# Optimization experiments

Measured on AMD Instinct MI355X. Metric: run time of the kernel, lower is better.

Reference implementation:

```python
import jax, jax.numpy as jnp
import numpy as np

K = 2            # top-k experts
TEMPERATURE = 1.0
EPS = 1e-9


def setup_inputs() -> dict:
    key = jax.random.key(0)
    k1, k2 = jax.random.split(key)
    B, S, D = 4, 4096, 4096
    G, E = 4, 64
    x = jax.random.normal(k1, (B, S, D), dtype=jnp.float32)
    # stacked gate weights, one [E, D] Linear weight per gate head
    W = jax.random.normal(k2, (G, E, D), dtype=jnp.float32) * 0.02
    return {"x": x, "W": W}


def reference(x, W):
    # per-head logits over experts: [B, S, G, E]; jitter disabled (eval / jitter_noise=0)
    logits = jnp.einsum('bsd,ged->bsge', x, W) * (1.0 / TEMPERATURE)
    probs = jax.nn.softmax(logits, axis=-1)          # softmax per head
    probs_full = probs.mean(axis=2)                  # consensus over heads: [B, S, E]
    topk_vals, idx = jax.lax.top_k(probs_full, K)    # sorted descending, matches aten.topk
    den = jnp.sum(topk_vals, axis=-1, keepdims=True)
    scores = topk_vals / jnp.maximum(den, EPS)       # clamp_min(den, 1e-9)
    pf = jax.lax.stop_gradient(probs_full)           # aux stats under no_grad
    importance = pf.mean(axis=(0, 1))                # [E]
    load = (pf > 0.0).astype(pf.dtype).mean(axis=(0, 1))  # [E]
    return idx, scores, probs_full, importance, load
```

## Files before the change

### kernel.cpp

```cpp
#include <hip/hip_runtime.h>

typedef _Float16 f16x8 __attribute__((ext_vector_type(8)));
typedef float    f32x4 __attribute__((ext_vector_type(4)));

#define MROWS 16384
#define NCOLS 256
#define KDIM  4096
#define BM    128
#define BK    32
#define LDA   40

#define OUT_SCORES 32768
#define OUT_PF     65536
#define OUT_IMP    1114112
#define OUT_LOAD   1114176

__global__ __launch_bounds__(256) void wprep(const float* __restrict__ W,
                                             _Float16* __restrict__ wfHi,
                                             _Float16* __restrict__ wfLo) {
    int t  = blockIdx.x * 256 + threadIdx.x;
    int n  = t >> 9;
    int k8 = t & 511;
    const float* src = W + ((size_t)n * KDIM + (size_t)k8 * 8);
    f16x8 hi, lo;
#pragma unroll
    for (int j = 0; j < 8; ++j) {
        float x = src[j];
        _Float16 h = (_Float16)x;
        hi[j] = h;
        lo[j] = (_Float16)(x - (float)h);
    }
    int NT  = n >> 4;
    int ksg = k8 >> 2;
    int l   = (n & 15) + ((k8 & 3) << 4);
    size_t dst = ((size_t)(ksg * 16 + NT) * 64 + (size_t)l) * 8;
    *(f16x8*)(wfHi + dst) = hi;
    *(f16x8*)(wfLo + dst) = lo;
}

__global__ __launch_bounds__(256, 2) void gemm3(const float* __restrict__ X,
        const _Float16* __restrict__ wfHi, const _Float16* __restrict__ wfLo,
        float* __restrict__ lsplit, int kQ) {
    __shared__ _Float16 aHi[BM * LDA];
    __shared__ _Float16 aLo[BM * LDA];

    const int tid  = threadIdx.x;
    const int lane = tid & 63;
    const int w    = tid >> 6;
    const int mt   = blockIdx.x & 127;
    const int s    = blockIdx.x >> 7;
    const int m0   = mt * BM;
    const int k0   = s * kQ;
    const int iters = kQ / BK;

    f32x4 acc[8][4];
#pragma unroll
    for (int a = 0; a < 8; ++a)
#pragma unroll
        for (int b = 0; b < 4; ++b) acc[a][b] = (f32x4){0.f, 0.f, 0.f, 0.f};

    const int sr = tid >> 1;
    const int sh = tid & 1;
    const float* xrow = X + ((size_t)(m0 + sr) * KDIM + (size_t)k0 + sh * 16);
    _Float16* wAH = aHi + sr * LDA + sh * 16;
    _Float16* wAL = aLo + sr * LDA + sh * 16;

    const _Float16* rAH = aHi + (lane & 15) * LDA + (lane >> 4) * 8;
    const _Float16* rAL = aLo + (lane & 15) * LDA + (lane >> 4) * 8;

    size_t bbase = (((size_t)(k0 >> 5) * 16 + (size_t)w * 4) * 64 + (size_t)lane) * 8;
    const _Float16* pBH = wfHi + bbase;
    const _Float16* pBL = wfLo + bbase;

    for (int i = 0; i < iters; ++i) {
        f16x8 bH[4], bL[4];
#pragma unroll
        for (int ni = 0; ni < 4; ++ni) {
            bH[ni] = *(const f16x8*)(pBH + (size_t)ni * 512);
            bL[ni] = *(const f16x8*)(pBL + (size_t)ni * 512);
        }
        pBH += 16 * 512;
        pBL += 16 * 512;

        float xv[16];
        const float* xp = xrow + (size_t)i * BK;
#pragma unroll
        for (int q = 0; q < 4; ++q) {
            f32x4 v = *(const f32x4*)(xp + q * 4);
            xv[q*4+0] = v[0]; xv[q*4+1] = v[1]; xv[q*4+2] = v[2]; xv[q*4+3] = v[3];
        }
        f16x8 h0, h1, l0, l1;
#pragma unroll
        for (int j = 0; j < 8; ++j) {
            _Float16 ha = (_Float16)xv[j];
            h0[j] = ha; l0[j] = (_Float16)(xv[j] - (float)ha);
            _Float16 hb = (_Float16)xv[8 + j];
            h1[j] = hb; l1[j] = (_Float16)(xv[8 + j] - (float)hb);
        }
        __syncthreads();
        *(f16x8*)(wAH)     = h0;
        *(f16x8*)(wAH + 8) = h1;
        *(f16x8*)(wAL)     = l0;
        *(f16x8*)(wAL + 8) = l1;
        __syncthreads();

#pragma unroll
        for (int mi = 0; mi < 8; ++mi) {
            f16x8 aH = *(const f16x8*)(rAH + mi * 16 * LDA);
            f16x8 aL = *(const f16x8*)(rAL + mi * 16 * LDA);
#pragma unroll
            for (int ni = 0; ni < 4; ++ni) {
                acc[mi][ni] = __builtin_amdgcn_mfma_f32_16x16x32_f16(aH, bH[ni], acc[mi][ni], 0, 0, 0);
                acc[mi][ni] = __builtin_amdgcn_mfma_f32_16x16x32_f16(aH, bL[ni], acc[mi][ni], 0, 0, 0);
                acc[mi][ni] = __builtin_amdgcn_mfma_f32_16x16x32_f16(aL, bH[ni], acc[mi][ni], 0, 0, 0);
            }
        }
    }

    float* outp = lsplit + (size_t)s * ((size_t)MROWS * NCOLS);
#pragma unroll
    for (int mi = 0; mi < 8; ++mi) {
#pragma unroll
        for (int ni = 0; ni < 4; ++ni) {
            int col   = w * 64 + ni * 16 + (lane & 15);
            int rbase = m0 + mi * 16 + ((lane >> 4) << 2);
#pragma unroll
            for (int r = 0; r < 4; ++r)
                outp[(size_t)(rbase + r) * NCOLS + col] = acc[mi][ni][r];
        }
    }
}

__global__ __launch_bounds__(256) void finalize(const float* __restrict__ lsplit,
                                                int nsplit, float* __restrict__ out) {
    __shared__ float sImp[64], sLoad[64];
    const int tid = threadIdx.x;
    if (tid < 64) { sImp[tid] = 0.f; sLoad[tid] = 0.f; }
    __syncthreads();

    const int i   = tid & 15;
    const int grp = tid >> 4;
    const int r   = blockIdx.x * 16 + grp;

    float v[16];
#pragma unroll
    for (int t = 0; t < 16; ++t) {
        size_t off = (size_t)r * 256 + (size_t)i + 16 * t;
        float a = lsplit[off];
        for (int s = 1; s < nsplit; ++s)
            a += lsplit[(size_t)s * ((size_t)MROWS * NCOLS) + off];
        v[t] = a;
    }

    float hm[4];
#pragma unroll
    for (int g = 0; g < 4; ++g) {
        float m = fmaxf(fmaxf(v[4*g], v[4*g+1]), fmaxf(v[4*g+2], v[4*g+3]));
#pragma unroll
        for (int msk = 1; msk < 16; msk <<= 1)
            m = fmaxf(m, __shfl_xor(m, msk));
        hm[g] = m;
    }
    float p[16], inv[4];
#pragma unroll
    for (int g = 0; g < 4; ++g) {
        float sa = 0.f;
#pragma unroll
        for (int q = 0; q < 4; ++q) { p[4*g+q] = __expf(v[4*g+q] - hm[g]); sa += p[4*g+q]; }
#pragma unroll
        for (int msk = 1; msk < 16; msk <<= 1)
            sa += __shfl_xor(sa, msk);
        inv[g] = 1.f / sa;
    }

    float pf[4];
#pragma unroll
    for (int et = 0; et < 4; ++et) {
        pf[et] = 0.25f * (p[et] * inv[0] + p[4+et] * inv[1] + p[8+et] * inv[2] + p[12+et] * inv[3]);
        out[OUT_PF + (size_t)r * 64 + i + 16 * et] = pf[et];
        atomicAdd(&sImp[i + 16 * et], pf[et]);
        atomicAdd(&sLoad[i + 16 * et], pf[et] > 0.f ? 1.f : 0.f);
    }

    float v1 = -3.4e38f, v2 = -3.4e38f; int e1 = 0, e2 = 0;
#pragma unroll
    for (int et = 0; et < 4; ++et) {
        int e = i + 16 * et; float val = pf[et];
        if (val > v1) { v2 = v1; e2 = e1; v1 = val; e1 = e; }
        else if (val > v2) { v2 = val; e2 = e; }
    }
#pragma unroll
    for (int msk = 1; msk < 16; msk <<= 1) {
        float o1 = __shfl_xor(v1, msk); int oe1 = __shfl_xor(e1, msk);
        float o2 = __shfl_xor(v2, msk); int oe2 = __shfl_xor(e2, msk);
        bool ob = (o1 > v1) || (o1 == v1 && oe1 < e1);
        if (ob) {
            bool vb = (v1 > o2) || (v1 == o2 && e1 < oe2);
            v2 = vb ? v1 : o2; e2 = vb ? e1 : oe2;
            v1 = o1; e1 = oe1;
        } else {
            bool nb = (o1 > v2) || (o1 == v2 && oe1 < e2);
            v2 = nb ? o1 : v2; e2 = nb ? oe1 : e2;
        }
    }
    if (i == 0) {
        float den = fmaxf(v1 + v2, 1e-9f);
        out[(size_t)r * 2]              = (float)e1;
        out[(size_t)r * 2 + 1]          = (float)e2;
        out[OUT_SCORES + (size_t)r * 2]     = v1 / den;
        out[OUT_SCORES + (size_t)r * 2 + 1] = v2 / den;
    }
    __syncthreads();
    if (tid < 64) {
        atomicAdd(out + OUT_IMP  + tid, sImp[tid]  * (1.0f / 16384.0f));
        atomicAdd(out + OUT_LOAD + tid, sLoad[tid] * (1.0f / 16384.0f));
    }
}

extern "C" void kernel_launch(void* const* d_in, const int* in_sizes, int n_in,
                              void* d_out, int out_size, void* d_ws, size_t ws_size,
                              hipStream_t stream) {
    const float* X = (const float*)d_in[0];
    const float* W = (const float*)d_in[1];
    float* out = (float*)d_out;
    char* ws = (char*)d_ws;

    _Float16* wfHi = (_Float16*)ws;
    _Float16* wfLo = (_Float16*)(ws + (2u << 20));
    float* lsplit  = (float*)(ws + (4u << 20));

    const size_t per = 16u << 20;
    int nsplit = (ws_size >= (4u << 20) + 4 * per) ? 4
               : (ws_size >= (4u << 20) + 2 * per) ? 2 : 1;

    hipMemsetAsync((void*)(out + OUT_IMP), 0, 128 * sizeof(float), stream);

    wprep<<<512, 256, 0, stream>>>(W, wfHi, wfLo);
    gemm3<<<128 * nsplit, 256, 0, stream>>>(X, wfHi, wfLo, lsplit, KDIM / nsplit);
    finalize<<<1024, 256, 0, stream>>>(lsplit, nsplit, out);
}
```

Baseline: 453.0 us.

## Double-buffer A tile in LDS and prefetch next X slice into registers

Doubles the LDS staging buffers for the split-f16 A tile so each iteration needs one barrier instead of two, and prefetches the next iteration's X values into registers while the current tile is processed. It also raises wave priority around the MFMA block with s_setprio. The goal is to hide global load latency and barrier stalls in the GEMM main loop. In exchange it uses twice the LDS and more registers per thread, which may reduce occupancy under the launch bound of 2 blocks per CU.

```diff
diff --git a/kernel.cpp b/kernel.cpp
--- a/kernel.cpp
+++ b/kernel.cpp
@@ -41,8 +41,8 @@
 __global__ __launch_bounds__(256, 2) void gemm3(const float* __restrict__ X,
         const _Float16* __restrict__ wfHi, const _Float16* __restrict__ wfLo,
         float* __restrict__ lsplit, int kQ) {
-    __shared__ _Float16 aHi[BM * LDA];
-    __shared__ _Float16 aLo[BM * LDA];
+    __shared__ _Float16 aHi[2][BM * LDA];
+    __shared__ _Float16 aLo[2][BM * LDA];
 
     const int tid  = threadIdx.x;
     const int lane = tid & 63;
@@ -62,16 +62,18 @@
     const int sr = tid >> 1;
     const int sh = tid & 1;
     const float* xrow = X + ((size_t)(m0 + sr) * KDIM + (size_t)k0 + sh * 16);
-    _Float16* wAH = aHi + sr * LDA + sh * 16;
-    _Float16* wAL = aLo + sr * LDA + sh * 16;
-
-    const _Float16* rAH = aHi + (lane & 15) * LDA + (lane >> 4) * 8;
-    const _Float16* rAL = aLo + (lane & 15) * LDA + (lane >> 4) * 8;
+    const int woff = sr * LDA + sh * 16;
+
+    const int roff = (lane & 15) * LDA + (lane >> 4) * 8;
 
     size_t bbase = (((size_t)(k0 >> 5) * 16 + (size_t)w * 4) * 64 + (size_t)lane) * 8;
     const _Float16* pBH = wfHi + bbase;
     const _Float16* pBL = wfLo + bbase;
 
+    f32x4 xq[4];
+#pragma unroll
+    for (int q = 0; q < 4; ++q) xq[q] = *(const f32x4*)(xrow + q * 4);
+
     for (int i = 0; i < iters; ++i) {
         f16x8 bH[4], bL[4];
 #pragma unroll
@@ -82,12 +84,18 @@
         pBH += 16 * 512;
         pBL += 16 * 512;
 
+        f32x4 xqN[4];
+        {
+            const float* xp = xrow + (size_t)((i + 1 < iters) ? (i + 1) : 0) * BK;
+#pragma unroll
+            for (int q = 0; q < 4; ++q) xqN[q] = *(const f32x4*)(xp + q * 4);
+        }
+
         float xv[16];
-        const float* xp = xrow + (size_t)i * BK;
 #pragma unroll
         for (int q = 0; q < 4; ++q) {
-            f32x4 v = *(const f32x4*)(xp + q * 4);
-            xv[q*4+0] = v[0]; xv[q*4+1] = v[1]; xv[q*4+2] = v[2]; xv[q*4+3] = v[3];
+            xv[q*4+0] = xq[q][0]; xv[q*4+1] = xq[q][1];
+            xv[q*4+2] = xq[q][2]; xv[q*4+3] = xq[q][3];
         }
         f16x8 h0, h1, l0, l1;
 #pragma unroll
@@ -97,13 +105,21 @@
             _Float16 hb = (_Float16)xv[8 + j];
             h1[j] = hb; l1[j] = (_Float16)(xv[8 + j] - (float)hb);
         }
-        __syncthreads();
+
+        _Float16* wAH = &aHi[i & 1][woff];
+        _Float16* wAL = &aLo[i & 1][woff];
         *(f16x8*)(wAH)     = h0;
         *(f16x8*)(wAH + 8) = h1;
         *(f16x8*)(wAL)     = l0;
         *(f16x8*)(wAL + 8) = l1;
-        __syncthreads();
-
+
+        asm volatile("s_waitcnt lgkmcnt(0)" ::: "memory");
+        __builtin_amdgcn_s_barrier();
+        __builtin_amdgcn_sched_barrier(0);
+
+        const _Float16* rAH = &aHi[i & 1][roff];
+        const _Float16* rAL = &aLo[i & 1][roff];
+        __builtin_amdgcn_s_setprio(1);
 #pragma unroll
         for (int mi = 0; mi < 8; ++mi) {
             f16x8 aH = *(const f16x8*)(rAH + mi * 16 * LDA);
@@ -115,6 +131,10 @@
                 acc[mi][ni] = __builtin_amdgcn_mfma_f32_16x16x32_f16(aL, bH[ni], acc[mi][ni], 0, 0, 0);
             }
         }
+        __builtin_amdgcn_s_setprio(0);
+
+#pragma unroll
+        for (int q = 0; q < 4; ++q) xq[q] = xqN[q];
     }
 
     float* outp = lsplit + (size_t)s * ((size_t)MROWS * NCOLS);
```

After: 450.6 us. Within noise of the previous version (-0.5%).
